# Kernel tuning notes

Measured on AMD Instinct MI355X. Metric: run time of the kernel, lower is better.

Reference implementation:

```python
import jax, jax.numpy as jnp
import numpy as np

N = 50000          # num nodes
E = 800000         # num edges
NUM_CLASSES = 40
FEAT_DIM = 256
FEAT_HID = 64
DEG_HID = 32
HID = 128
IN_CH = NUM_CLASSES + FEAT_HID + DEG_HID  # 136
MAX_DEG = 256      # degree-embedding table size (clip; random graph max deg << 256)


def _init_linear(key, fan_in, fan_out):
    kw, kb = jax.random.split(key)
    s = 1.0 / np.sqrt(fan_in)
    W = jax.random.uniform(kw, (fan_in, fan_out), jnp.float32, -s, s)
    b = jax.random.uniform(kb, (fan_out,), jnp.float32, -s, s)
    return W, b


def setup_inputs() -> dict:
    key = jax.random.key(0)
    ks = jax.random.split(key, 8)
    logits = jax.random.normal(ks[0], (N, NUM_CLASSES), jnp.float32)
    features = jax.random.normal(ks[1], (N, FEAT_DIM), jnp.float32)
    edge_index = jax.random.randint(ks[2], (2, E), 0, N, jnp.int32)
    Wf, bf = _init_linear(ks[3], FEAT_DIM, FEAT_HID)
    deg_table = jax.random.normal(ks[4], (MAX_DEG, DEG_HID), jnp.float32)
    W1, b1 = _init_linear(ks[5], IN_CH, HID)
    W2, b2 = _init_linear(ks[6], HID, HID)
    W3, b3 = _init_linear(ks[7], HID, NUM_CLASSES)
    return {"logits": logits, "features": features, "edge_index": edge_index,
            "Wf": Wf, "bf": bf, "deg_table": deg_table,
            "W1": W1, "b1": b1, "W2": W2, "b2": b2, "W3": W3, "b3": b3}


def reference(logits, features, edge_index, Wf, bf, deg_table, W1, b1, W2, b2, W3, b3):
    src, dst = edge_index[0], edge_index[1]
    # degree embedding: deg = degree(src) + degree(dst) on original edges
    ones_e = jnp.ones(src.shape[0], logits.dtype)
    deg = jax.ops.segment_sum(ones_e, src, num_segments=N) + \
          jax.ops.segment_sum(ones_e, dst, num_segments=N)
    deg_idx = jnp.clip(deg.astype(jnp.int32), 0, MAX_DEG - 1)
    deg_emb = deg_table[deg_idx]                              # [N, DEG_HID]

    x = jnp.concatenate([logits, features @ Wf + bf, deg_emb], axis=-1)  # [N, 136]

    # GCN normalization with self-loops (PyG gcn_norm): deg from dst column
    loop = jnp.arange(N, dtype=src.dtype)
    s = jnp.concatenate([src, loop])
    d = jnp.concatenate([dst, loop])
    dg = jax.ops.segment_sum(jnp.ones(d.shape[0], x.dtype), d, num_segments=N)
    dinv = jnp.where(dg > 0, jax.lax.rsqrt(dg), 0.0)
    norm = dinv[s] * dinv[d]                                  # [E+N]

    def conv(h, W, b):
        h = h @ W                                             # linear first
        msg = h[s] * norm[:, None]                            # gather + scale
        return jax.ops.segment_sum(msg, d, num_segments=N) + b

    x = jax.nn.relu(conv(x, W1, b1))   # dropout identity (inference)
    x = jax.nn.relu(conv(x, W2, b2))
    return conv(x, W3, b3)             # [N, NUM_CLASSES]
```

## Files before the change

kernel.cpp:

```cpp
#include <hip/hip_runtime.h>
#include <hip/hip_bf16.h>

constexpr int cN = 50000;
constexpr int cE = 800000;
constexpr int cNUM_CLASSES = 40;
constexpr int cFEAT_DIM = 256;
constexpr int cFEAT_HID = 64;
constexpr int cDEG_HID = 32;
constexpr int cHID = 128;
constexpr int cMAX_DEG = 256;
constexpr int cKF = 352;

constexpr int cNCHUNK = 128;
constexpr int cCHUNK  = cE / cNCHUNK;
constexpr int cWORDS  = cN / 2;
constexpr int cHWORDS = cWORDS / 2;
constexpr int cSCANB  = (cWORDS + 255) / 256;

typedef unsigned short ushort8_t __attribute__((ext_vector_type(8)));
typedef short short8_t __attribute__((ext_vector_type(8)));
typedef float float4_t __attribute__((ext_vector_type(4)));

__device__ __forceinline__ unsigned short f2bf(float f) {
    unsigned u = __builtin_bit_cast(unsigned, f);
    u += 0x7fff + ((u >> 16) & 1);
    return (unsigned short)(u >> 16);
}
__device__ __forceinline__ float bf2f(unsigned short s) {
    unsigned u = ((unsigned)s) << 16;
    return __builtin_bit_cast(float, u);
}

__global__ __launch_bounds__(256) void prep_kernel(const int* __restrict__ edge,
                                                   unsigned* __restrict__ partial,
                                                   const float* __restrict__ Wf,
                                                   const float* __restrict__ bfv,
                                                   const float* __restrict__ W1,
                                                   const float* __restrict__ W2,
                                                   const float* __restrict__ W3,
                                                   unsigned short* __restrict__ Btc,
                                                   unsigned short* __restrict__ Wt2,
                                                   unsigned short* __restrict__ Wt3,
                                                   float* __restrict__ bias2) {
    __shared__ unsigned lds[cHWORDS];
    const int b = blockIdx.x, tid = threadIdx.x;
    if (b < 512) {
        const int cb = b & (cNCHUNK - 1);
        const int half = (b >> 7) & 1;
        const int which = b >> 8;
        for (int i = tid; i < cHWORDS; i += 256) lds[i] = 0;
        __syncthreads();
        const int* ids = edge + (size_t)which * cE + (size_t)cb * cCHUNK;
        const int lo = half * (cN / 2), hi = lo + cN / 2;
        const int wbase = half * cHWORDS;
        for (int i = tid; i < cCHUNK; i += 256) {
            int v = ids[i];
            if (v >= lo && v < hi)
                atomicAdd(&lds[(v >> 1) - wbase], 1u << ((v & 1) * 16));
        }
        __syncthreads();
        unsigned* outp = partial + ((size_t)which * cNCHUNK + cb) * cWORDS + wbase;
        for (int i = tid; i < cHWORDS; i += 256) outp[i] = lds[i];
        return;
    }
    if (b < 648) {
        int i = (b - 512) * 256 + tid;
        if (i < 12288) {
            int n = i / 96, r = i - (i / 96) * 96;
            unsigned short v;
            if (r < 40)       v = f2bf(W1[r * cHID + n]);
            else if (r < 72)  v = f2bf(W1[(104 + r - 40) * cHID + n]);
            else              v = 0;
            int k = (r < 40) ? r : (r < 72 ? 296 + (r - 40) : 328 + (r - 72));
            Btc[n * cKF + k] = v;
            return;
        }
        i -= 12288;
        if (i < 16384) {
            int n = i >> 7, k = i & 127;
            Wt2[n * cHID + k] = f2bf(W2[k * cHID + n]);
            return;
        }
        i -= 16384;
        if (i < 6144) {
            int n = i >> 7, k = i & 127;
            Wt3[n * cHID + k] = (n < cNUM_CLASSES) ? f2bf(W3[k * cNUM_CLASSES + n]) : 0;
        }
        return;
    }
    if (b < 776) {
        int i = (b - 648) * 256 + tid;
        int kf = i >> 7, n = i & 127;
        float s = 0.f;
        #pragma unroll 8
        for (int j = 0; j < cFEAT_HID; ++j)
            s += Wf[kf * cFEAT_HID + j] * W1[(40 + j) * cHID + n];
        Btc[n * cKF + 40 + kf] = f2bf(s);
        return;
    }
    if (tid < cHID) {
        float s = 0.f;
        #pragma unroll 8
        for (int j = 0; j < cFEAT_HID; ++j)
            s += bfv[j] * W1[(40 + j) * cHID + tid];
        bias2[tid] = s;
    }
}

__global__ __launch_bounds__(256) void mega_scan_kernel(unsigned* __restrict__ partial,
                                                        int* __restrict__ rowptr,
                                                        float* __restrict__ dinv,
                                                        int* __restrict__ degidx,
                                                        int* __restrict__ desc) {
    const int b = blockIdx.x, tid = threadIdx.x;
    const int w = b * 256 + tid;
    unsigned slo = 0, shi = 0, plo = 0, phi = 0;
    if (w < cWORDS) {
        const unsigned* ps = partial + w;
        for (int c = 0; c < cNCHUNK; ++c) {
            unsigned v = ps[(size_t)c * cWORDS];
            slo += v & 0xFFFFu; shi += v >> 16;
        }
        unsigned* pd = partial + (size_t)cNCHUNK * cWORDS + w;
        for (int c = 0; c < cNCHUNK; ++c) {
            unsigned v = pd[(size_t)c * cWORDS];
            pd[(size_t)c * cWORDS] = plo | (phi << 16);
            plo += v & 0xFFFFu; phi += v >> 16;
        }
        int d0 = (int)(slo + plo), d1 = (int)(shi + phi);
        degidx[2 * w]     = d0 > cMAX_DEG - 1 ? cMAX_DEG - 1 : d0;
        degidx[2 * w + 1] = d1 > cMAX_DEG - 1 ? cMAX_DEG - 1 : d1;
    }
    __shared__ int s[256];
    int tot = (int)(plo + phi);
    s[tid] = tot;
    __syncthreads();
    #pragma unroll
    for (int off = 1; off < 256; off <<= 1) {
        int t = (tid >= off) ? s[tid - off] : 0;
        __syncthreads();
        s[tid] += t;
        __syncthreads();
    }
    int ex_local = s[tid] - tot;
    int block_total = s[255];
    if (tid == 0) atomicExch(&desc[b], block_total + 1);
    if (tid < b) {
        int v;
        do { v = atomicAdd(&desc[tid], 0); } while (v == 0);
        s[tid] = v - 1;
    }
    __syncthreads();
    if (tid >= b) s[tid] = 0;
    __syncthreads();
    #pragma unroll
    for (int off = 128; off > 0; off >>= 1) {
        if (tid < off) s[tid] += s[tid + off];
        __syncthreads();
    }
    int base = s[0] + ex_local;
    if (w < cWORDS) {
        rowptr[2 * w]     = base;
        rowptr[2 * w + 1] = base + (int)plo;
        dinv[2 * w]     = rsqrtf((float)(plo + 1));
        dinv[2 * w + 1] = rsqrtf((float)(phi + 1));
    }
    if (b == 0 && tid == 0) rowptr[cN] = cE;
}

__global__ __launch_bounds__(256) void scatter2_kernel(const int* __restrict__ edge,
                                                       const unsigned* __restrict__ partial,
                                                       const int* __restrict__ rowptr,
                                                       int* __restrict__ adj) {
    __shared__ unsigned lds[cHWORDS];
    const int b = blockIdx.x, tid = threadIdx.x;
    const int cb = b & (cNCHUNK - 1);
    const int half = b >> 7;
    const int wbase = half * cHWORDS;
    const unsigned* pp = partial + ((size_t)cNCHUNK + cb) * cWORDS + wbase;
    for (int i = tid; i < cHWORDS; i += 256) lds[i] = pp[i];
    __syncthreads();
    const int* srcs = edge + (size_t)cb * cCHUNK;
    const int* dsts = edge + cE + (size_t)cb * cCHUNK;
    const int lo = half * (cN / 2), hi = lo + cN / 2;
    for (int i = tid; i < cCHUNK; i += 256) {
        int d = dsts[i];
        if (d >= lo && d < hi) {
            int sh = (d & 1) * 16;
            unsigned old = atomicAdd(&lds[(d >> 1) - wbase], 1u << sh);
            int off = (int)((old >> sh) & 0xFFFFu);
            adj[rowptr[d] + off] = srcs[i];
        }
    }
}

__global__ __launch_bounds__(256) void gemm_fused(const float* __restrict__ logits,
                                                  const float* __restrict__ features,
                                                  const float* __restrict__ deg_table,
                                                  const int* __restrict__ degidx,
                                                  const unsigned short* __restrict__ Btc,
                                                  const float* __restrict__ bias2,
                                                  unsigned short* __restrict__ out) {
    constexpr int NT = 8;
    __shared__ unsigned short As[64 * 32];
    __shared__ unsigned short Bs[NT * 16 * 32];

    const int tid = threadIdx.x;
    const int wave = tid >> 6;
    const int lane = tid & 63;
    const int m15 = lane & 15;
    const int q = lane >> 4;
    const int rowbase = blockIdx.x * 64;

    float4_t acc[NT];
    #pragma unroll
    for (int t = 0; t < NT; ++t) acc[t] = (float4_t){0.f, 0.f, 0.f, 0.f};

    const int arow = tid >> 2;
    const int akq = (tid & 3) * 8;
    int gr = rowbase + arow;
    if (gr > cN - 1) gr = cN - 1;
    const int didx = degidx[gr];

    for (int k0 = 0; k0 < cKF; k0 += 32) {
        #pragma unroll
        for (int h = 0; h < 2; ++h) {
            int k4 = k0 + akq + h * 4;
            float4 v = make_float4(0.f, 0.f, 0.f, 0.f);
            if (k4 < 40)       v = *(const float4*)&logits[(size_t)gr * cNUM_CLASSES + k4];
            else if (k4 < 296) v = *(const float4*)&features[(size_t)gr * cFEAT_DIM + (k4 - 40)];
            else if (k4 < 328) v = *(const float4*)&deg_table[didx * cDEG_HID + (k4 - 296)];
            unsigned short* dst = &As[arow * 32 + akq + h * 4];
            dst[0] = f2bf(v.x); dst[1] = f2bf(v.y); dst[2] = f2bf(v.z); dst[3] = f2bf(v.w);
        }
        for (int i = tid; i < NT * 64; i += 256) {
            int n = i >> 2;
            int kq = (i & 3) * 8;
            *(ushort8_t*)&Bs[n * 32 + kq] = *(const ushort8_t*)&Btc[(size_t)n * cKF + k0 + kq];
        }
        __syncthreads();

        short8_t a = *(const short8_t*)&As[(wave * 16 + m15) * 32 + q * 8];
        #pragma unroll
        for (int t = 0; t < NT; ++t) {
            short8_t bfr = *(const short8_t*)&Bs[(t * 16 + m15) * 32 + q * 8];
            acc[t] = __builtin_amdgcn_mfma_f32_16x16x32_bf16(a, bfr, acc[t], 0, 0, 0);
        }
        __syncthreads();
    }

    #pragma unroll
    for (int t = 0; t < NT; ++t) {
        int col = t * 16 + m15;
        float bv = bias2[col];
        #pragma unroll
        for (int r = 0; r < 4; ++r) {
            int row = rowbase + wave * 16 + q * 4 + r;
            if (row < cN)
                out[(size_t)row * cHID + col] = f2bf(acc[t][r] + bv);
        }
    }
}

template <int KTOT, int NT, int OSTR, int OUTC>
__global__ __launch_bounds__(256) void mfma_gemm(const unsigned short* __restrict__ A,
                                                 const unsigned short* __restrict__ Bt,
                                                 unsigned short* __restrict__ out) {
    __shared__ unsigned short As[64 * 32];
    __shared__ unsigned short Bs[NT * 16 * 32];

    const int tid = threadIdx.x;
    const int wave = tid >> 6;
    const int lane = tid & 63;
    const int m15 = lane & 15;
    const int q = lane >> 4;
    const int rowbase = blockIdx.x * 64;

    float4_t acc[NT];
    #pragma unroll
    for (int t = 0; t < NT; ++t) acc[t] = (float4_t){0.f, 0.f, 0.f, 0.f};

    const int arow = tid >> 2;
    const int akq = (tid & 3) * 8;
    int gr = rowbase + arow;
    if (gr > cN - 1) gr = cN - 1;

    for (int k0 = 0; k0 < KTOT; k0 += 32) {
        *(ushort8_t*)&As[arow * 32 + akq] =
            *(const ushort8_t*)&A[(size_t)gr * KTOT + k0 + akq];
        for (int i = tid; i < NT * 64; i += 256) {
            int n = i >> 2;
            int kq = (i & 3) * 8;
            *(ushort8_t*)&Bs[n * 32 + kq] = *(const ushort8_t*)&Bt[(size_t)n * KTOT + k0 + kq];
        }
        __syncthreads();

        short8_t a = *(const short8_t*)&As[(wave * 16 + m15) * 32 + q * 8];
        #pragma unroll
        for (int t = 0; t < NT; ++t) {
            short8_t b = *(const short8_t*)&Bs[(t * 16 + m15) * 32 + q * 8];
            acc[t] = __builtin_amdgcn_mfma_f32_16x16x32_bf16(a, b, acc[t], 0, 0, 0);
        }
        __syncthreads();
    }

    #pragma unroll
    for (int t = 0; t < NT; ++t) {
        int col = t * 16 + m15;
        if (OUTC % 16 != 0 && col >= OUTC) continue;
        #pragma unroll
        for (int r = 0; r < 4; ++r) {
            int row = rowbase + wave * 16 + q * 4 + r;
            if (row < cN)
                out[(size_t)row * OSTR + col] = f2bf(acc[t][r]);
        }
    }
}

template <bool RELU>
__global__ __launch_bounds__(128) void agg_bf128(const unsigned short* __restrict__ t,
                                                 const int* __restrict__ rowptr,
                                                 const int* __restrict__ adj,
                                                 const float* __restrict__ dinv,
                                                 const float* __restrict__ b,
                                                 unsigned short* __restrict__ outb) {
    const int tid = threadIdx.x;
    const int lane = tid & 15;
    const int row = blockIdx.x * 8 + (tid >> 4);
    if (row >= cN) return;
    const int c = lane * 8;
    const float di = dinv[row];
    int e = rowptr[row];
    const int end = rowptr[row + 1];
    float a0[8], a1[8];
    #pragma unroll
    for (int k = 0; k < 8; ++k) { a0[k] = 0.f; a1[k] = 0.f; }
    for (; e + 1 < end; e += 2) {
        int j0 = adj[e], j1 = adj[e + 1];
        float v0 = dinv[j0], v1 = dinv[j1];
        ushort8_t t0 = *(const ushort8_t*)&t[(size_t)j0 * cHID + c];
        ushort8_t t1 = *(const ushort8_t*)&t[(size_t)j1 * cHID + c];
        #pragma unroll
        for (int k = 0; k < 8; ++k) {
            a0[k] += v0 * bf2f(t0[k]);
            a1[k] += v1 * bf2f(t1[k]);
        }
    }
    if (e < end) {
        int j0 = adj[e];
        float v0 = dinv[j0];
        ushort8_t t0 = *(const ushort8_t*)&t[(size_t)j0 * cHID + c];
        #pragma unroll
        for (int k = 0; k < 8; ++k) a0[k] += v0 * bf2f(t0[k]);
    }
    ushort8_t ts = *(const ushort8_t*)&t[(size_t)row * cHID + c];
    const float d2 = di * di;
    ushort8_t o;
    #pragma unroll
    for (int k = 0; k < 8; ++k) {
        float r = di * (a0[k] + a1[k]) + d2 * bf2f(ts[k]) + b[c + k];
        if (RELU) r = fmaxf(r, 0.f);
        o[k] = f2bf(r);
    }
    *(ushort8_t*)&outb[(size_t)row * cHID + c] = o;
}

__global__ __launch_bounds__(128) void agg_bf40(const unsigned short* __restrict__ t,
                                                const int* __restrict__ rowptr,
                                                const int* __restrict__ adj,
                                                const float* __restrict__ dinv,
                                                const float* __restrict__ b,
                                                float* __restrict__ out) {
    const int tid = threadIdx.x;
    const int lane = tid & 7;
    const int row = blockIdx.x * 16 + (tid >> 3);
    if (row >= cN) return;
    const int c = lane * 8;
    if (c >= cNUM_CLASSES) return;
    const float di = dinv[row];
    int e = rowptr[row];
    const int end = rowptr[row + 1];
    float a0[8], a1[8];
    #pragma unroll
    for (int k = 0; k < 8; ++k) { a0[k] = 0.f; a1[k] = 0.f; }
    for (; e + 1 < end; e += 2) {
        int j0 = adj[e], j1 = adj[e + 1];
        float v0 = dinv[j0], v1 = dinv[j1];
        ushort8_t t0 = *(const ushort8_t*)&t[(size_t)j0 * cNUM_CLASSES + c];
        ushort8_t t1 = *(const ushort8_t*)&t[(size_t)j1 * cNUM_CLASSES + c];
        #pragma unroll
        for (int k = 0; k < 8; ++k) {
            a0[k] += v0 * bf2f(t0[k]);
            a1[k] += v1 * bf2f(t1[k]);
        }
    }
    if (e < end) {
        int j0 = adj[e];
        float v0 = dinv[j0];
        ushort8_t t0 = *(const ushort8_t*)&t[(size_t)j0 * cNUM_CLASSES + c];
        #pragma unroll
        for (int k = 0; k < 8; ++k) a0[k] += v0 * bf2f(t0[k]);
    }
    ushort8_t ts = *(const ushort8_t*)&t[(size_t)row * cNUM_CLASSES + c];
    const float d2 = di * di;
    float r[8];
    #pragma unroll
    for (int k = 0; k < 8; ++k) r[k] = di * (a0[k] + a1[k]) + d2 * bf2f(ts[k]) + b[c + k];
    float4 v0 = make_float4(r[0], r[1], r[2], r[3]);
    float4 v1 = make_float4(r[4], r[5], r[6], r[7]);
    *(float4*)&out[(size_t)row * cNUM_CLASSES + c] = v0;
    *(float4*)&out[(size_t)row * cNUM_CLASSES + c + 4] = v1;
}

extern "C" void kernel_launch(void* const* d_in, const int* in_sizes, int n_in,
                              void* d_out, int out_size, void* d_ws, size_t ws_size,
                              hipStream_t stream) {
    const float* logits    = (const float*)d_in[0];
    const float* features  = (const float*)d_in[1];
    const int*   edge      = (const int*)d_in[2];
    const float* Wf        = (const float*)d_in[3];
    const float* bfv       = (const float*)d_in[4];
    const float* deg_table = (const float*)d_in[5];
    const float* W1        = (const float*)d_in[6];
    const float* b1        = (const float*)d_in[7];
    const float* W2        = (const float*)d_in[8];
    const float* b2        = (const float*)d_in[9];
    const float* W3        = (const float*)d_in[10];
    const float* b3        = (const float*)d_in[11];
    float* out = (float*)d_out;

    int* rowptr    = (int*)d_ws;
    int* adj       = rowptr + cN + 16;
    int* desc      = adj + cE;
    int* degidx    = desc + 128;
    float* dinv    = (float*)(degidx + cN);
    float* bias2   = dinv + cN;
    unsigned short* tb  = (unsigned short*)(bias2 + 128);
    unsigned short* hb  = tb + (size_t)cN * cHID;
    unsigned short* Btc = hb + (size_t)cN * cHID;
    unsigned short* Wt2 = Btc + 128 * cKF;
    unsigned short* Wt3 = Wt2 + 128 * cHID;
    unsigned* partial = (unsigned*)(Wt3 + 48 * cHID);

    hipMemsetAsync(desc, 0, 128 * sizeof(int), stream);

    prep_kernel<<<777, 256, 0, stream>>>(edge, partial, Wf, bfv, W1, W2, W3,
                                         Btc, Wt2, Wt3, bias2);

    mega_scan_kernel<<<cSCANB, 256, 0, stream>>>(partial, rowptr, dinv, degidx, desc);

    scatter2_kernel<<<256, 256, 0, stream>>>(edge, partial, rowptr, adj);

    constexpr int MB = (cN + 63) / 64;

    gemm_fused<<<MB, 256, 0, stream>>>(logits, features, deg_table, degidx, Btc, bias2, tb);
    agg_bf128<true><<<(cN + 7) / 8, 128, 0, stream>>>(tb, rowptr, adj, dinv, b1, hb);

    mfma_gemm<cHID, 8, cHID, cHID><<<MB, 256, 0, stream>>>(hb, Wt2, tb);
    agg_bf128<true><<<(cN + 7) / 8, 128, 0, stream>>>(tb, rowptr, adj, dinv, b2, hb);

    mfma_gemm<cHID, 3, cNUM_CLASSES, cNUM_CLASSES><<<MB, 256, 0, stream>>>(hb, Wt3, tb);
    agg_bf40<<<(cN + 15) / 16, 128, 0, stream>>>(tb, rowptr, adj, dinv, b3, out);
}
```

Measured before the change: 293.5 us.

## Fuse CSR scatter with first GEMM, halve histogram chunks, drop memset

Merges the adjacency scatter kernel and the fused first-layer GEMM into one launch: the first 128 blocks build the CSR adjacency and the rest run the GEMM, sharing a single LDS buffer. The histogram chunk count drops from 128 to 64, so there are fewer partial-count blocks and less partial data for the scan to sum. The hipMemsetAsync for the scan descriptors is replaced by zeroing inside prep_kernel. This removes two launches and lets the scatter overlap with GEMM work, but each scatter block now processes twice as many edges, which lengthens its critical path.

```diff
diff --git a/kernel.cpp b/kernel.cpp
--- a/kernel.cpp
+++ b/kernel.cpp
@@ -11,7 +11,7 @@
 constexpr int cMAX_DEG = 256;
 constexpr int cKF = 352;
 
-constexpr int cNCHUNK = 128;
+constexpr int cNCHUNK = 64;
 constexpr int cCHUNK  = cE / cNCHUNK;
 constexpr int cWORDS  = cN / 2;
 constexpr int cHWORDS = cWORDS / 2;
@@ -41,13 +41,14 @@
                                                    unsigned short* __restrict__ Btc,
                                                    unsigned short* __restrict__ Wt2,
                                                    unsigned short* __restrict__ Wt3,
-                                                   float* __restrict__ bias2) {
+                                                   float* __restrict__ bias2,
+                                                   int* __restrict__ desc) {
     __shared__ unsigned lds[cHWORDS];
     const int b = blockIdx.x, tid = threadIdx.x;
-    if (b < 512) {
+    if (b < 256) {
         const int cb = b & (cNCHUNK - 1);
-        const int half = (b >> 7) & 1;
-        const int which = b >> 8;
+        const int half = (b >> 6) & 1;
+        const int which = b >> 7;
         for (int i = tid; i < cHWORDS; i += 256) lds[i] = 0;
         __syncthreads();
         const int* ids = edge + (size_t)which * cE + (size_t)cb * cCHUNK;
@@ -63,8 +64,8 @@
         for (int i = tid; i < cHWORDS; i += 256) outp[i] = lds[i];
         return;
     }
-    if (b < 648) {
-        int i = (b - 512) * 256 + tid;
+    if (b < 392) {
+        int i = (b - 256) * 256 + tid;
         if (i < 12288) {
             int n = i / 96, r = i - (i / 96) * 96;
             unsigned short v;
@@ -88,8 +89,8 @@
         }
         return;
     }
-    if (b < 776) {
-        int i = (b - 648) * 256 + tid;
+    if (b < 456) {
+        int i = (b - 392) * 256 + tid;
         int kf = i >> 7, n = i & 127;
         float s = 0.f;
         #pragma unroll 8
@@ -104,6 +105,8 @@
         for (int j = 0; j < cFEAT_HID; ++j)
             s += bfv[j] * W1[(40 + j) * cHID + tid];
         bias2[tid] = s;
+    } else if (tid - 128 < cSCANB) {
+        desc[tid - 128] = 0;
     }
 }
 
@@ -168,49 +171,52 @@
     if (b == 0 && tid == 0) rowptr[cN] = cE;
 }
 
-__global__ __launch_bounds__(256) void scatter2_kernel(const int* __restrict__ edge,
-                                                       const unsigned* __restrict__ partial,
-                                                       const int* __restrict__ rowptr,
-                                                       int* __restrict__ adj) {
-    __shared__ unsigned lds[cHWORDS];
+__global__ __launch_bounds__(256) void scatter_gemm_kernel(const int* __restrict__ edge,
+                                                           const unsigned* __restrict__ partial,
+                                                           const int* __restrict__ rowptr,
+                                                           int* __restrict__ adj,
+                                                           const float* __restrict__ logits,
+                                                           const float* __restrict__ features,
+                                                           const float* __restrict__ deg_table,
+                                                           const int* __restrict__ degidx,
+                                                           const unsigned short* __restrict__ Btc,
+                                                           const float* __restrict__ bias2,
+                                                           unsigned short* __restrict__ out) {
+    __shared__ unsigned shmem[cHWORDS];
     const int b = blockIdx.x, tid = threadIdx.x;
-    const int cb = b & (cNCHUNK - 1);
-    const int half = b >> 7;
-    const int wbase = half * cHWORDS;
-    const unsigned* pp = partial + ((size_t)cNCHUNK + cb) * cWORDS + wbase;
-    for (int i = tid; i < cHWORDS; i += 256) lds[i] = pp[i];
-    __syncthreads();
-    const int* srcs = edge + (size_t)cb * cCHUNK;
-    const int* dsts = edge + cE + (size_t)cb * cCHUNK;
-    const int lo = half * (cN / 2), hi = lo + cN / 2;
-    for (int i = tid; i < cCHUNK; i += 256) {
-        int d = dsts[i];
-        if (d >= lo && d < hi) {
-            int sh = (d & 1) * 16;
-            unsigned old = atomicAdd(&lds[(d >> 1) - wbase], 1u << sh);
-            int off = (int)((old >> sh) & 0xFFFFu);
-            adj[rowptr[d] + off] = srcs[i];
-        }
-    }
-}
-
-__global__ __launch_bounds__(256) void gemm_fused(const float* __restrict__ logits,
-                                                  const float* __restrict__ features,
-                                                  const float* __restrict__ deg_table,
-                                                  const int* __restrict__ degidx,
-                                                  const unsigned short* __restrict__ Btc,
-                                                  const float* __restrict__ bias2,
-                                                  unsigned short* __restrict__ out) {
+
+    if (b < 128) {
+        const int cb = b & (cNCHUNK - 1);
+        const int half = (b >> 6) & 1;
+        const int wbase = half * cHWORDS;
+        const unsigned* pp = partial + ((size_t)cNCHUNK + cb) * cWORDS + wbase;
+        for (int i = tid; i < cHWORDS; i += 256) shmem[i] = pp[i];
+        __syncthreads();
+        const int* srcs = edge + (size_t)cb * cCHUNK;
+        const int* dsts = edge + cE + (size_t)cb * cCHUNK;
+        const int lo = half * (cN / 2), hi = lo + cN / 2;
+        for (int i = tid; i < cCHUNK; i += 256) {
+            int d = dsts[i];
+            if (d >= lo && d < hi) {
+                int sh = (d & 1) * 16;
+                unsigned old = atomicAdd(&shmem[(d >> 1) - wbase], 1u << sh);
+                int off = (int)((old >> sh) & 0xFFFFu);
+                adj[rowptr[d] + off] = srcs[i];
+            }
+        }
+        return;
+    }
+
     constexpr int NT = 8;
-    __shared__ unsigned short As[64 * 32];
-    __shared__ unsigned short Bs[NT * 16 * 32];
-
-    const int tid = threadIdx.x;
+    unsigned short* As = (unsigned short*)shmem;
+    unsigned short* Bs = As + 64 * 32;
+
+    const int gb = b - 128;
     const int wave = tid >> 6;
     const int lane = tid & 63;
     const int m15 = lane & 15;
     const int q = lane >> 4;
-    const int rowbase = blockIdx.x * 64;
+    const int rowbase = gb * 64;
 
     float4_t acc[NT];
     #pragma unroll
@@ -442,18 +448,16 @@
     unsigned short* Wt3 = Wt2 + 128 * cHID;
     unsigned* partial = (unsigned*)(Wt3 + 48 * cHID);
 
-    hipMemsetAsync(desc, 0, 128 * sizeof(int), stream);
-
-    prep_kernel<<<777, 256, 0, stream>>>(edge, partial, Wf, bfv, W1, W2, W3,
-                                         Btc, Wt2, Wt3, bias2);
+    prep_kernel<<<457, 256, 0, stream>>>(edge, partial, Wf, bfv, W1, W2, W3,
+                                         Btc, Wt2, Wt3, bias2, desc);
 
     mega_scan_kernel<<<cSCANB, 256, 0, stream>>>(partial, rowptr, dinv, degidx, desc);
 
-    scatter2_kernel<<<256, 256, 0, stream>>>(edge, partial, rowptr, adj);
-
     constexpr int MB = (cN + 63) / 64;
 
-    gemm_fused<<<MB, 256, 0, stream>>>(logits, features, deg_table, degidx, Btc, bias2, tb);
+    scatter_gemm_kernel<<<128 + MB, 256, 0, stream>>>(edge, partial, rowptr, adj,
+                                                      logits, features, deg_table, degidx,
+                                                      Btc, bias2, tb);
     agg_bf128<true><<<(cN + 7) / 8, 128, 0, stream>>>(tb, rowptr, adj, dinv, b1, hb);
 
     mfma_gemm<cHID, 8, cHID, cHID><<<MB, 256, 0, stream>>>(hb, Wt2, tb);
```

After: 287.5 us. 1.02x faster.
